# Optimization experiments

Hardware: AMD Instinct MI355X
Metric: run time of the kernel (lower is better)

## Reference

```python
import jax, jax.numpy as jnp
import numpy as np

B, L, D = 64, 1024, 1024


def _attn(q, K, V, mask):
    # q: [B,D], K/V: [B,L,D], mask: [B,L] bool (True = valid)
    scores = jnp.einsum('bd,bld->bl', q, K) / jnp.sqrt(jnp.asarray(D, q.dtype))
    scores = jnp.where(mask, scores, -jnp.inf)
    attn = jax.nn.softmax(scores, axis=-1)
    attn = jnp.where(jnp.isnan(attn), 0.0, attn)  # torch.nan_to_num for all-masked rows
    return jnp.einsum('bl,bld->bd', attn, V)


def setup_inputs() -> dict:
    key = jax.random.key(0)
    ks = jax.random.split(key, 12)
    xav = float(np.sqrt(6.0 / (D + D)))  # xavier_uniform for square Linear
    img_mask = jax.random.randint(ks[4], (B, L), 0, 2).astype(bool)
    txt_mask = jax.random.randint(ks[7], (B, L), 0, 2).astype(bool)
    # guarantee at least one valid token per row
    img_mask = img_mask.at[:, 0].set(True)
    txt_mask = txt_mask.at[:, 0].set(True)
    return {
        'img_q': jax.random.normal(ks[0], (B, D), jnp.float32),
        'txt_q': jax.random.normal(ks[1], (B, D), jnp.float32),
        'K_img': jax.random.normal(ks[2], (B, L, D), jnp.float32),
        'V_img': jax.random.normal(ks[3], (B, L, D), jnp.float32),
        'img_mask': img_mask,
        'K_txt': jax.random.normal(ks[5], (B, L, D), jnp.float32),
        'V_txt': jax.random.normal(ks[6], (B, L, D), jnp.float32),
        'txt_mask': txt_mask,
        'W_img': jax.random.uniform(ks[8], (D, D), jnp.float32, -xav, xav),
        'b_img': jnp.zeros((D,), jnp.float32),
        'W_txt': jax.random.uniform(ks[9], (D, D), jnp.float32, -xav, xav),
        'b_txt': jnp.zeros((D,), jnp.float32),
    }


def reference(img_q, txt_q, K_img, V_img, img_mask, K_txt, V_txt, txt_mask,
              W_img, b_img, W_txt, b_txt):
    # Dropout is identity in eval mode.
    ctx_img = _attn(txt_q, K_img, V_img, img_mask)
    img_q = img_q + ctx_img @ W_img.T + b_img
    ctx_txt = _attn(img_q, K_txt, V_txt, txt_mask)
    txt_q = txt_q + ctx_txt @ W_txt.T + b_txt
    return (img_q, txt_q)
```

## Files before the change

kernel.cpp:

```cpp
#include <hip/hip_runtime.h>
#include <hip/hip_bf16.h>
#include <float.h>

#define B_ 64
#define L_ 1024
#define D_ 1024
#define NSPLIT 8
#define CHUNK 128
#define PSTRIDE 1028

typedef __bf16 bf16x8 __attribute__((ext_vector_type(8)));
typedef float f32x4 __attribute__((ext_vector_type(4)));

__device__ inline unsigned short f2bf(float x) {
    unsigned int u = __float_as_uint(x);
    unsigned int lsb = (u >> 16) & 1u;
    u += 0x7fffu + lsb;
    return (unsigned short)(u >> 16);
}

__global__ __launch_bounds__(512, 2) void attn_kernel(
    const float* __restrict__ q,
    const float* __restrict__ K,
    const float* __restrict__ V,
    const int*   __restrict__ mask,
    float* __restrict__ part,
    const float* __restrict__ cs0,
    const float* __restrict__ cs1,
    unsigned short* __restrict__ cd0,
    unsigned short* __restrict__ cd1,
    int nattn)
{
    const int tid = threadIdx.x;

    if ((int)blockIdx.x >= nattn) {
        int i = ((int)blockIdx.x - nattn) * 512 + tid;
        float4 v0 = reinterpret_cast<const float4*>(cs0)[i];
        float4 v1 = reinterpret_cast<const float4*>(cs1)[i];
        ushort4 u0, u1;
        u0.x = f2bf(v0.x); u0.y = f2bf(v0.y); u0.z = f2bf(v0.z); u0.w = f2bf(v0.w);
        u1.x = f2bf(v1.x); u1.y = f2bf(v1.y); u1.z = f2bf(v1.z); u1.w = f2bf(v1.w);
        reinterpret_cast<ushort4*>(cd0)[i] = u0;
        reinterpret_cast<ushort4*>(cd1)[i] = u1;
        return;
    }

    const int bid  = blockIdx.x;
    const int b    = bid >> 3;
    const int sp   = bid & 7;
    const int l0   = sp * CHUNK;
    const int wave = tid >> 6;
    const int lane = tid & 63;

    __shared__ int   vidx[CHUNK];
    __shared__ float sc[CHUNK];
    __shared__ float pw[CHUNK];
    __shared__ int   nvalid;

    const float4* qptr = reinterpret_cast<const float4*>(q + (size_t)b * D_);
    float4 qreg[4];
    #pragma unroll
    for (int rep = 0; rep < 4; ++rep) qreg[rep] = qptr[lane + rep * 64];

    if (wave == 0) {
        const int* mp = mask + (size_t)b * L_ + l0;
        int mv0 = mp[lane];
        int mv1 = mp[64 + lane];
        unsigned long long bal0 = __ballot(mv0 != 0);
        unsigned long long bal1 = __ballot(mv1 != 0);
        int n0 = __popcll(bal0);
        int nv = n0 + __popcll(bal1);
        unsigned long long lt = (1ull << lane) - 1;
        if (mv0) vidx[__popcll(bal0 & lt)] = lane;
        if (mv1) vidx[n0 + __popcll(bal1 & lt)] = 64 + lane;
        int padv = bal0 ? (__ffsll((long long)bal0) - 1)
                        : (bal1 ? 64 + __ffsll((long long)bal1) - 1 : 0);
        if (nv + lane < CHUNK) vidx[nv + lane] = padv;
        if (lane == 0) nvalid = nv;
    }
    __syncthreads();
    const int nv    = nvalid;
    const int nvp8  = (nv + 7)  & ~7;
    const int nvp16 = (nv + 15) & ~15;

    const float* Kb = K + ((size_t)b * L_ + l0) * D_;
    for (int jj = wave; jj < nvp16; jj += 16) {
        int j2 = jj + 8;
        const float4* k0 = reinterpret_cast<const float4*>(Kb + vidx[jj] * D_);
        const float4* k1 = reinterpret_cast<const float4*>(Kb + vidx[j2] * D_);
        float4 kv0[4], kv1[4];
        #pragma unroll
        for (int rep = 0; rep < 4; ++rep) { kv0[rep] = k0[lane + rep * 64];
                                            kv1[rep] = k1[lane + rep * 64]; }
        float a0a = 0.f, a0b = 0.f, a1a = 0.f, a1b = 0.f;
        #pragma unroll
        for (int rep = 0; rep < 4; rep += 2) {
            a0a += kv0[rep].x * qreg[rep].x + kv0[rep].y * qreg[rep].y
                 + kv0[rep].z * qreg[rep].z + kv0[rep].w * qreg[rep].w;
            a0b += kv0[rep+1].x * qreg[rep+1].x + kv0[rep+1].y * qreg[rep+1].y
                 + kv0[rep+1].z * qreg[rep+1].z + kv0[rep+1].w * qreg[rep+1].w;
            a1a += kv1[rep].x * qreg[rep].x + kv1[rep].y * qreg[rep].y
                 + kv1[rep].z * qreg[rep].z + kv1[rep].w * qreg[rep].w;
            a1b += kv1[rep+1].x * qreg[rep+1].x + kv1[rep+1].y * qreg[rep+1].y
                 + kv1[rep+1].z * qreg[rep+1].z + kv1[rep+1].w * qreg[rep+1].w;
        }
        float a0 = a0a + a0b, a1 = a1a + a1b;
        #pragma unroll
        for (int off = 32; off > 0; off >>= 1) {
            a0 += __shfl_xor(a0, off, 64);
            a1 += __shfl_xor(a1, off, 64);
        }
        if (lane == 0) { sc[jj] = a0 * 0.03125f; sc[j2] = a1 * 0.03125f; }
    }
    __syncthreads();

    if (tid < CHUNK) pw[tid] = (tid < nv) ? __expf(sc[tid]) : 0.f;
    __syncthreads();

    float se = 0.f, ax = 0.f, ay = 0.f;
    const float2* vbase = reinterpret_cast<const float2*>(V + ((size_t)b * L_ + l0) * D_);
    for (int j = 0; j < nvp8; j += 8) {
        float p[8]; int ix[8];
        #pragma unroll
        for (int t = 0; t < 8; ++t) { p[t] = pw[j + t]; ix[t] = vidx[j + t]; }
        float2 vv[8];
        #pragma unroll
        for (int t = 0; t < 8; ++t) vv[t] = vbase[ix[t] * (D_ / 2) + tid];
        #pragma unroll
        for (int t = 0; t < 8; ++t) {
            se += p[t];
            ax += p[t] * vv[t].x; ay += p[t] * vv[t].y;
        }
    }

    float* po = part + (size_t)bid * PSTRIDE;
    float2 o; o.x = ax; o.y = ay;
    reinterpret_cast<float2*>(po)[tid] = o;
    if (tid == 0) po[D_] = se;
}

__global__ __launch_bounds__(256) void combine_kernel(
    const float* __restrict__ part,
    unsigned short* __restrict__ ctxb)
{
    const int b   = blockIdx.x;
    const int tid = threadIdx.x;
    const float* pb = part + (size_t)b * NSPLIT * PSTRIDE;

    float denom = 0.f;
    #pragma unroll
    for (int s = 0; s < NSPLIT; ++s) denom += pb[(size_t)s * PSTRIDE + D_];
    float inv = 1.f / denom;

    float ax = 0.f, ay = 0.f, az = 0.f, aw = 0.f;
    #pragma unroll
    for (int s = 0; s < NSPLIT; ++s) {
        float4 o = reinterpret_cast<const float4*>(pb + (size_t)s * PSTRIDE)[tid];
        ax += o.x; ay += o.y; az += o.z; aw += o.w;
    }
    ushort4 u;
    u.x = f2bf(ax * inv); u.y = f2bf(ay * inv);
    u.z = f2bf(az * inv); u.w = f2bf(aw * inv);
    reinterpret_cast<ushort4*>(ctxb)[(size_t)b * (D_ / 4) + tid] = u;
}

__global__ __launch_bounds__(256) void proj_kernel(
    const unsigned short* __restrict__ Abf,
    const unsigned short* __restrict__ Wbf,
    const float* __restrict__ qin,
    const float* __restrict__ bias,
    float* __restrict__ out)
{
    const int tid  = threadIdx.x;
    const int wave = tid >> 6;
    const int lane = tid & 63;
    const int m0   = (blockIdx.x & 3) * 16;
    const int n0   = (blockIdx.x >> 2) * 16;
    const int r    = lane & 15;
    const int g    = lane >> 4;

    const bf16x8* aptr = reinterpret_cast<const bf16x8*>(
        Abf + (size_t)(m0 + r) * D_ + g * 8 + wave * 256);
    const bf16x8* bptr = reinterpret_cast<const bf16x8*>(
        Wbf + (size_t)(n0 + r) * D_ + g * 8 + wave * 256);

    f32x4 acc = {0.f, 0.f, 0.f, 0.f};
    #pragma unroll
    for (int kk = 0; kk < 8; ++kk) {
        bf16x8 a  = aptr[kk * 4];
        bf16x8 bb = bptr[kk * 4];
        acc = __builtin_amdgcn_mfma_f32_16x16x32_bf16(a, bb, acc, 0, 0, 0);
    }

    __shared__ float red[1024];
    #pragma unroll
    for (int i = 0; i < 4; ++i) red[wave * 256 + lane * 4 + i] = acc[i];
    __syncthreads();

    int ol = tid >> 2, oi = tid & 3;
    float v = red[ol * 4 + oi] + red[256 + ol * 4 + oi]
            + red[512 + ol * 4 + oi] + red[768 + ol * 4 + oi];
    int row = m0 + ((ol >> 4) * 4 + oi);
    int col = n0 + (ol & 15);
    out[(size_t)row * D_ + col] = qin[(size_t)row * D_ + col] + bias[col] + v;
}

extern "C" void kernel_launch(void* const* d_in, const int* in_sizes, int n_in,
                              void* d_out, int out_size, void* d_ws, size_t ws_size,
                              hipStream_t stream) {
    const float* img_q    = (const float*)d_in[0];
    const float* txt_q    = (const float*)d_in[1];
    const float* K_img    = (const float*)d_in[2];
    const float* V_img    = (const float*)d_in[3];
    const int*   img_mask = (const int*)  d_in[4];
    const float* K_txt    = (const float*)d_in[5];
    const float* V_txt    = (const float*)d_in[6];
    const int*   txt_mask = (const int*)  d_in[7];
    const float* W_img    = (const float*)d_in[8];
    const float* b_img    = (const float*)d_in[9];
    const float* W_txt    = (const float*)d_in[10];
    const float* b_txt    = (const float*)d_in[11];

    float* out_img = (float*)d_out;
    float* out_txt = (float*)d_out + B_ * D_;

    char* ws = (char*)d_ws;
    float* part = (float*)ws;
    size_t part_bytes = (size_t)B_ * NSPLIT * PSTRIDE * sizeof(float);
    unsigned short* Wimg_bf = (unsigned short*)(ws + part_bytes);
    unsigned short* Wtxt_bf = Wimg_bf + (size_t)D_ * D_;
    unsigned short* ctx_bf  = Wtxt_bf + (size_t)D_ * D_;

    attn_kernel<<<1024, 512, 0, stream>>>(
        txt_q, K_img, V_img, img_mask, part,
        W_img, W_txt, Wimg_bf, Wtxt_bf, B_ * NSPLIT);
    combine_kernel<<<B_, 256, 0, stream>>>(part, ctx_bf);
    proj_kernel<<<256, 256, 0, stream>>>(ctx_bf, Wimg_bf, img_q, b_img, out_img);
    attn_kernel<<<512, 512, 0, stream>>>(
        out_img, K_txt, V_txt, txt_mask, part,
        nullptr, nullptr, nullptr, nullptr, B_ * NSPLIT);
    combine_kernel<<<B_, 256, 0, stream>>>(part, ctx_bf);
    proj_kernel<<<256, 256, 0, stream>>>(ctx_bf, Wtxt_bf, txt_q, b_txt, out_txt);
}
```

Measured before the change: 124.0 us.

## Fuse score and PV phases per wave with cross-wave LDS reduction

Each wave now processes one valid key row at a time, computing its dot product with q, exponentiating, and immediately accumulating p*V for the whole D dimension in registers. Per-wave partial outputs are then reduced across the 8 waves through LDS. This removes the separate score, exp and PV phases along with their two block barriers, and lets K and V loads for a row be issued together. In exchange it adds a 32 KB LDS reduction buffer, higher register use, and one K row in flight per wave instead of two.

```diff
diff --git a/kernel.cpp b/kernel.cpp
--- a/kernel.cpp
+++ b/kernel.cpp
@@ -52,10 +52,10 @@
     const int wave = tid >> 6;
     const int lane = tid & 63;
 
-    __shared__ int   vidx[CHUNK];
-    __shared__ float sc[CHUNK];
-    __shared__ float pw[CHUNK];
-    __shared__ int   nvalid;
+    __shared__ int    vidx[CHUNK];
+    __shared__ int    nvalid;
+    __shared__ float4 ored[8 * 256];
+    __shared__ float  sered[8];
 
     const float4* qptr = reinterpret_cast<const float4*>(q + (size_t)b * D_);
     float4 qreg[4];
@@ -79,64 +79,68 @@
         if (lane == 0) nvalid = nv;
     }
     __syncthreads();
-    const int nv    = nvalid;
-    const int nvp8  = (nv + 7)  & ~7;
-    const int nvp16 = (nv + 15) & ~15;
+    const int nv   = nvalid;
+    const int nvp8 = (nv + 7) & ~7;
 
     const float* Kb = K + ((size_t)b * L_ + l0) * D_;
-    for (int jj = wave; jj < nvp16; jj += 16) {
-        int j2 = jj + 8;
-        const float4* k0 = reinterpret_cast<const float4*>(Kb + vidx[jj] * D_);
-        const float4* k1 = reinterpret_cast<const float4*>(Kb + vidx[j2] * D_);
-        float4 kv0[4], kv1[4];
-        #pragma unroll
-        for (int rep = 0; rep < 4; ++rep) { kv0[rep] = k0[lane + rep * 64];
-                                            kv1[rep] = k1[lane + rep * 64]; }
-        float a0a = 0.f, a0b = 0.f, a1a = 0.f, a1b = 0.f;
-        #pragma unroll
-        for (int rep = 0; rep < 4; rep += 2) {
-            a0a += kv0[rep].x * qreg[rep].x + kv0[rep].y * qreg[rep].y
-                 + kv0[rep].z * qreg[rep].z + kv0[rep].w * qreg[rep].w;
-            a0b += kv0[rep+1].x * qreg[rep+1].x + kv0[rep+1].y * qreg[rep+1].y
-                 + kv0[rep+1].z * qreg[rep+1].z + kv0[rep+1].w * qreg[rep+1].w;
-            a1a += kv1[rep].x * qreg[rep].x + kv1[rep].y * qreg[rep].y
-                 + kv1[rep].z * qreg[rep].z + kv1[rep].w * qreg[rep].w;
-            a1b += kv1[rep+1].x * qreg[rep+1].x + kv1[rep+1].y * qreg[rep+1].y
-                 + kv1[rep+1].z * qreg[rep+1].z + kv1[rep+1].w * qreg[rep+1].w;
+    const float* Vb = V + ((size_t)b * L_ + l0) * D_;
+
+    float4 o0 = {0,0,0,0}, o1 = {0,0,0,0}, o2 = {0,0,0,0}, o3 = {0,0,0,0};
+    float se = 0.f;
+
+    for (int j = wave; j < nvp8; j += 8) {
+        int row = vidx[j];
+        const float4* kr = reinterpret_cast<const float4*>(Kb + row * D_);
+        const float4* vr = reinterpret_cast<const float4*>(Vb + row * D_);
+        float4 kv[4], vv[4];
+        #pragma unroll
+        for (int rep = 0; rep < 4; ++rep) kv[rep] = kr[lane + rep * 64];
+        #pragma unroll
+        for (int rep = 0; rep < 4; ++rep) vv[rep] = vr[lane + rep * 64];
+
+        float aa = kv[0].x * qreg[0].x + kv[0].y * qreg[0].y
+                 + kv[0].z * qreg[0].z + kv[0].w * qreg[0].w
+                 + kv[2].x * qreg[2].x + kv[2].y * qreg[2].y
+                 + kv[2].z * qreg[2].z + kv[2].w * qreg[2].w;
+        float ab = kv[1].x * qreg[1].x + kv[1].y * qreg[1].y
+                 + kv[1].z * qreg[1].z + kv[1].w * qreg[1].w
+                 + kv[3].x * qreg[3].x + kv[3].y * qreg[3].y
+                 + kv[3].z * qreg[3].z + kv[3].w * qreg[3].w;
+        float s = aa + ab;
+        #pragma unroll
+        for (int off = 32; off > 0; off >>= 1) s += __shfl_xor(s, off, 64);
+
+        float p = (j < nv) ? __expf(s * 0.03125f) : 0.f;
+        se += p;
+        o0.x += p * vv[0].x; o0.y += p * vv[0].y; o0.z += p * vv[0].z; o0.w += p * vv[0].w;
+        o1.x += p * vv[1].x; o1.y += p * vv[1].y; o1.z += p * vv[1].z; o1.w += p * vv[1].w;
+        o2.x += p * vv[2].x; o2.y += p * vv[2].y; o2.z += p * vv[2].z; o2.w += p * vv[2].w;
+        o3.x += p * vv[3].x; o3.y += p * vv[3].y; o3.z += p * vv[3].z; o3.w += p * vv[3].w;
+    }
+
+    ored[wave * 256 + lane      ] = o0;
+    ored[wave * 256 + lane +  64] = o1;
+    ored[wave * 256 + lane + 128] = o2;
+    ored[wave * 256 + lane + 192] = o3;
+    if (lane == 0) sered[wave] = se;
+    __syncthreads();
+
+    float* po = part + (size_t)bid * PSTRIDE;
+    if (tid < 256) {
+        float4 acc = ored[tid];
+        #pragma unroll
+        for (int w = 1; w < 8; ++w) {
+            float4 v = ored[w * 256 + tid];
+            acc.x += v.x; acc.y += v.y; acc.z += v.z; acc.w += v.w;
         }
-        float a0 = a0a + a0b, a1 = a1a + a1b;
-        #pragma unroll
-        for (int off = 32; off > 0; off >>= 1) {
-            a0 += __shfl_xor(a0, off, 64);
-            a1 += __shfl_xor(a1, off, 64);
-        }
-        if (lane == 0) { sc[jj] = a0 * 0.03125f; sc[j2] = a1 * 0.03125f; }
-    }
-    __syncthreads();
-
-    if (tid < CHUNK) pw[tid] = (tid < nv) ? __expf(sc[tid]) : 0.f;
-    __syncthreads();
-
-    float se = 0.f, ax = 0.f, ay = 0.f;
-    const float2* vbase = reinterpret_cast<const float2*>(V + ((size_t)b * L_ + l0) * D_);
-    for (int j = 0; j < nvp8; j += 8) {
-        float p[8]; int ix[8];
-        #pragma unroll
-        for (int t = 0; t < 8; ++t) { p[t] = pw[j + t]; ix[t] = vidx[j + t]; }
-        float2 vv[8];
-        #pragma unroll
-        for (int t = 0; t < 8; ++t) vv[t] = vbase[ix[t] * (D_ / 2) + tid];
-        #pragma unroll
-        for (int t = 0; t < 8; ++t) {
-            se += p[t];
-            ax += p[t] * vv[t].x; ay += p[t] * vv[t].y;
-        }
-    }
-
-    float* po = part + (size_t)bid * PSTRIDE;
-    float2 o; o.x = ax; o.y = ay;
-    reinterpret_cast<float2*>(po)[tid] = o;
-    if (tid == 0) po[D_] = se;
+        reinterpret_cast<float4*>(po)[tid] = acc;
+    }
+    if (tid == 0) {
+        float t = 0.f;
+        #pragma unroll
+        for (int w = 0; w < 8; ++w) t += sered[w];
+        po[D_] = t;
+    }
 }
 
 __global__ __launch_bounds__(256) void combine_kernel(
```

Measured after the change: 125.6 us. About the same (+1.3%).
